# Kernel tuning notes

Measured on AMD Instinct MI355X. Metric: run time of the kernel, lower is better.

Reference implementation:

```python
import jax, jax.numpy as jnp
import numpy as np

N_HEADS = 32
N_KV_HEADS = 8
HEAD_DIM = 128
ROPE_BASE = 10000.0
NEG_INF = -1e9


def rope(x, base=ROPE_BASE, offset=0):
    # x: [B, H, L, d]; 'traditional' RoPE with the module's rotation formula.
    d = x.shape[-1]
    t = jnp.arange(x.shape[2], dtype=jnp.float32) + offset
    freqs = base ** (-jnp.arange(0, d, 2, dtype=jnp.float32) / d)  # [d/2]
    ang = t[:, None] * freqs[None, :]                              # [L, d/2]
    cos, sin = jnp.cos(ang), jnp.sin(ang)
    x1, x2 = x[..., 0::2], x[..., 1::2]
    out = jnp.stack([x1 * cos + x2 * sin, x1 * sin - x2 * cos], axis=-1)
    return out.reshape(x.shape)


def setup_inputs() -> dict:
    key = jax.random.key(0)
    ks = jax.random.split(key, 5)
    B, L, D = 2, 2048, 4096
    x = jax.random.normal(ks[0], (B, L, D), dtype=jnp.float32)
    wq = jax.random.normal(ks[1], (D, N_HEADS * HEAD_DIM), dtype=jnp.float32) * 0.02
    wk = jax.random.normal(ks[2], (D, N_KV_HEADS * HEAD_DIM), dtype=jnp.float32) * 0.02
    wv = jax.random.normal(ks[3], (D, N_KV_HEADS * HEAD_DIM), dtype=jnp.float32) * 0.02
    wo = jax.random.normal(ks[4], (N_HEADS * HEAD_DIM, D), dtype=jnp.float32) * 0.02
    # causal additive mask [L, L]
    mask = jnp.where(jnp.tril(jnp.ones((L, L), dtype=bool)), 0.0, NEG_INF).astype(jnp.float32)
    return {"x": x, "mask": mask, "wq": wq, "wk": wk, "wv": wv, "wo": wo}


def reference(x, mask, wq, wk, wv, wo):
    B, L, D = x.shape
    scale = HEAD_DIM ** -0.5
    q = (x @ wq).reshape(B, L, N_HEADS, HEAD_DIM).transpose(0, 2, 1, 3)     # [B,H,L,d]
    k = (x @ wk).reshape(B, L, N_KV_HEADS, HEAD_DIM).transpose(0, 2, 1, 3)  # [B,Hk,L,d]
    v = (x @ wv).reshape(B, L, N_KV_HEADS, HEAD_DIM).transpose(0, 2, 1, 3)
    rep = N_HEADS // N_KV_HEADS
    k = jnp.repeat(k, rep, axis=1)  # [B,H,L,d]  (physical GQA repeat, as in source)
    v = jnp.repeat(v, rep, axis=1)
    q = rope(q)
    k = rope(k)
    scores = jnp.einsum("bhqd,bhkd->bhqk", q * scale, k) + mask  # [B,H,L,L]
    probs = jax.nn.softmax(scores.astype(jnp.float32), axis=-1).astype(scores.dtype)
    out = jnp.einsum("bhqk,bhkd->bhqd", probs, v)
    out = out.transpose(0, 2, 1, 3).reshape(B, L, N_HEADS * HEAD_DIM)
    return out @ wo, (k, v)
```

## Files before the change

kernel.cpp:

```cpp
#include <hip/hip_runtime.h>

typedef unsigned short u16;
typedef unsigned int u32;
typedef float f32x4 __attribute__((ext_vector_type(4)));
typedef u32 u32x2 __attribute__((ext_vector_type(2)));
typedef __bf16 bf16x8 __attribute__((ext_vector_type(8)));

#define DEV __device__ __forceinline__

DEV u16 f2b(float f) {
    union { float f; u32 u; } v; v.f = f;
    u32 r = v.u + 0x7fffu + ((v.u >> 16) & 1u);
    return (u16)(r >> 16);
}
DEV float b2f(u16 b) {
    union { u32 u; float f; } v; v.u = ((u32)b) << 16;
    return v.f;
}

DEV void gload16(const void* g, void* l) {
    __builtin_amdgcn_global_load_lds((const __attribute__((address_space(1))) void*)g,
                                     (__attribute__((address_space(3))) void*)l, 16, 0, 0);
}

DEV f32x4 mfma16(bf16x8 a, bf16x8 b, f32x4 c) {
    return __builtin_amdgcn_mfma_f32_16x16x32_bf16(a, b, c, 0, 0, 0);
}

__global__ __launch_bounds__(256) void convx_kernel(const float* __restrict__ in,
                                                    u16* __restrict__ out) {
    size_t i = ((size_t)blockIdx.x * 256 + threadIdx.x) * 4;
    float4 v = *(const float4*)(in + i);
    ushort4 o; o.x = f2b(v.x); o.y = f2b(v.y); o.z = f2b(v.z); o.w = f2b(v.w);
    *(ushort4*)(out + i) = o;
}

__global__ __launch_bounds__(256) void tconv_kernel(const float* __restrict__ in,
                                                    u16* __restrict__ out, int K, int N) {
    __shared__ float tile[64][65];
    int t = threadIdx.x;
    int n0 = blockIdx.x * 64, k0 = blockIdx.y * 64;
    int r = t >> 4, c4 = (t & 15) * 4;
#pragma unroll
    for (int i = 0; i < 4; ++i) {
        float4 v = *(const float4*)(in + (size_t)(k0 + i * 16 + r) * N + n0 + c4);
        tile[i * 16 + r][c4 + 0] = v.x; tile[i * 16 + r][c4 + 1] = v.y;
        tile[i * 16 + r][c4 + 2] = v.z; tile[i * 16 + r][c4 + 3] = v.w;
    }
    __syncthreads();
#pragma unroll
    for (int i = 0; i < 4; ++i) {
        int nn = i * 16 + r;
        ushort4 o;
        o.x = f2b(tile[c4 + 0][nn]); o.y = f2b(tile[c4 + 1][nn]);
        o.z = f2b(tile[c4 + 2][nn]); o.w = f2b(tile[c4 + 3][nn]);
        *(ushort4*)(out + (size_t)(n0 + nn) * K + k0 + c4) = o;
    }
}

template <bool F32OUT>
__global__ __launch_bounds__(256, 2) void gemm128_kernel(const u16* __restrict__ A,
                                                         const u16* __restrict__ Bt,
                                                         u16* __restrict__ Cb,
                                                         float* __restrict__ Cf,
                                                         int N, int K, int gy) {
    __shared__ __align__(16) u16 Asb[2][2][64 * 64];
    __shared__ __align__(16) u16 Bsb[2][2][64 * 64];
    int t = threadIdx.x;
    int lane = t & 63, w = t >> 6;
    int wrM = w >> 1, wcN = w & 1;
    int lr = lane & 15, hi = lane >> 4;
    int wg = blockIdx.x;
    int swz = (wg & 7) * ((int)gridDim.x >> 3) + (wg >> 3);
    int bx = swz / gy, by = swz % gy;
    int m0 = by * 128, n0 = bx * 128;
    int nk = K >> 6;

    auto stageA = [&](int X, int h) {
        const u16* src = A + (size_t)(m0 + h * 64) * K + X * 64;
        char* dst = (char*)&Asb[X & 1][h][0];
#pragma unroll
        for (int it = 0; it < 2; ++it) {
            int c = it * 256 + t;
            int row = c >> 3;
            int col8 = ((c & 7) ^ (row & 7)) << 3;
            gload16(src + (size_t)row * K + col8, dst + (it * 256 + (t & ~63)) * 16);
        }
    };
    auto stageB = [&](int X, int h) {
        const u16* src = Bt + (size_t)(n0 + h * 64) * K + X * 64;
        char* dst = (char*)&Bsb[X & 1][h][0];
#pragma unroll
        for (int it = 0; it < 2; ++it) {
            int c = it * 256 + t;
            int row = c >> 3;
            int col8 = ((c & 7) ^ (row & 7)) << 3;
            gload16(src + (size_t)row * K + col8, dst + (it * 256 + (t & ~63)) * 16);
        }
    };

    stageA(0, 0); stageA(0, 1); stageB(0, 0); stageB(0, 1);
    stageA(1, 0); stageA(1, 1);
    asm volatile("s_waitcnt vmcnt(4)" ::: "memory");
    __builtin_amdgcn_s_barrier();

    f32x4 acc[4][4] = {};
    for (int kt = 0; kt < nk; ++kt) {
        __builtin_amdgcn_sched_barrier(0);
        int p = kt & 1;
        const char* Ah = (const char*)&Asb[p][wrM][0];
        const char* Bh = (const char*)&Bsb[p][wcN][0];
        bool s1 = (kt + 1 < nk), s2 = (kt + 2 < nk);
        bf16x8 a[4][2], bb[2][2];

#pragma unroll
        for (int mf = 0; mf < 4; ++mf)
#pragma unroll
            for (int ks = 0; ks < 2; ++ks) {
                int row = mf * 16 + lr;
                a[mf][ks] = *(const bf16x8*)(Ah + ((row * 128 + ks * 64 + hi * 16) ^ ((row & 7) << 4)));
            }
#pragma unroll
        for (int nf = 0; nf < 2; ++nf)
#pragma unroll
            for (int ks = 0; ks < 2; ++ks) {
                int row = nf * 16 + lr;
                bb[nf][ks] = *(const bf16x8*)(Bh + ((row * 128 + ks * 64 + hi * 16) ^ ((row & 7) << 4)));
            }
        if (s1) { stageB(kt + 1, 0); stageB(kt + 1, 1); }
        __builtin_amdgcn_s_barrier();
        __builtin_amdgcn_s_setprio(1);
#pragma unroll
        for (int mf = 0; mf < 4; ++mf)
#pragma unroll
            for (int nf = 0; nf < 2; ++nf)
#pragma unroll
                for (int ks = 0; ks < 2; ++ks)
                    acc[mf][nf] = mfma16(a[mf][ks], bb[nf][ks], acc[mf][nf]);
        __builtin_amdgcn_s_setprio(0);
        __builtin_amdgcn_s_barrier();

#pragma unroll
        for (int nf = 0; nf < 2; ++nf)
#pragma unroll
            for (int ks = 0; ks < 2; ++ks) {
                int row = (nf + 2) * 16 + lr;
                bb[nf][ks] = *(const bf16x8*)(Bh + ((row * 128 + ks * 64 + hi * 16) ^ ((row & 7) << 4)));
            }
        if (s2) { stageA(kt + 2, 0); stageA(kt + 2, 1); }
        __builtin_amdgcn_s_barrier();
        __builtin_amdgcn_s_setprio(1);
#pragma unroll
        for (int mf = 0; mf < 4; ++mf)
#pragma unroll
            for (int nf = 0; nf < 2; ++nf)
#pragma unroll
                for (int ks = 0; ks < 2; ++ks)
                    acc[mf][nf + 2] = mfma16(a[mf][ks], bb[nf][ks], acc[mf][nf + 2]);
        __builtin_amdgcn_s_setprio(0);
        if (s2)      asm volatile("s_waitcnt vmcnt(4)" ::: "memory");
        else if (s1) asm volatile("s_waitcnt vmcnt(0)" ::: "memory");
        __builtin_amdgcn_s_barrier();
    }

#pragma unroll
    for (int mf = 0; mf < 4; ++mf)
#pragma unroll
        for (int nf = 0; nf < 4; ++nf)
#pragma unroll
            for (int r = 0; r < 4; ++r) {
                int m = m0 + wrM * 64 + mf * 16 + hi * 4 + r;
                int n = n0 + wcN * 64 + nf * 16 + lr;
                if (F32OUT) Cf[(size_t)m * N + n] = acc[mf][nf][r];
                else        Cb[(size_t)m * N + n] = f2b(acc[mf][nf][r]);
            }
}

__global__ __launch_bounds__(256) void rope_kernel(u16* __restrict__ qkv,
                                                   float* __restrict__ outk) {
    int row = blockIdx.y;
    int p = blockIdx.x * 256 + threadIdx.x;
    int b = row >> 11, l = row & 2047;
    float freq = exp2f((float)(p & 63) * -0.2076205059304601f);
    float sv, cv; sincosf((float)l * freq, &sv, &cv);
    if (p < 2048) {
        int h = p >> 6, i = p & 63;
        size_t idx = (size_t)row * 6144 + h * 128 + 2 * i;
        u32 pr = *(const u32*)(qkv + idx);
        float x1 = b2f((u16)(pr & 0xffff)), x2 = b2f((u16)(pr >> 16));
        float o1 = x1 * cv + x2 * sv, o2 = x1 * sv - x2 * cv;
        *(u32*)(qkv + idx) = (u32)f2b(o1) | ((u32)f2b(o2) << 16);
    } else {
        int kvh = (p >> 6) - 32, i = p & 63;
        size_t idx = (size_t)row * 6144 + 4096 + kvh * 128 + 2 * i;
        u32 pr = *(const u32*)(qkv + idx);
        float x1 = b2f((u16)(pr & 0xffff)), x2 = b2f((u16)(pr >> 16));
        float o1 = x1 * cv + x2 * sv, o2 = x1 * sv - x2 * cv;
        *(u32*)(qkv + idx) = (u32)f2b(o1) | ((u32)f2b(o2) << 16);
#pragma unroll
        for (int r = 0; r < 4; ++r) {
            float2 o; o.x = o1; o.y = o2;
            *(float2*)(outk + ((size_t)((b * 32 + kvh * 4 + r) * 2048) + l) * 128 + 2 * i) = o;
        }
    }
}

__global__ __launch_bounds__(256) void vtrans_kernel(const u16* __restrict__ qkv,
                                                     u16* __restrict__ vt,
                                                     float* __restrict__ outv) {
    __shared__ u16 tile[64][65];
    int t = threadIdx.x;
    int l0 = blockIdx.x * 64, d0 = blockIdx.y * 64;
    int z = blockIdx.z, b = z >> 3, kvh = z & 7;
    int r = t >> 4, c4 = (t & 15) * 4;
#pragma unroll
    for (int i = 0; i < 4; ++i) {
        int l = l0 + i * 16 + r;
        ushort4 v = *(const ushort4*)(qkv + (size_t)(b * 2048 + l) * 6144 + 5120 + kvh * 128 + d0 + c4);
        tile[i * 16 + r][c4 + 0] = v.x; tile[i * 16 + r][c4 + 1] = v.y;
        tile[i * 16 + r][c4 + 2] = v.z; tile[i * 16 + r][c4 + 3] = v.w;
        float4 f; f.x = b2f(v.x); f.y = b2f(v.y); f.z = b2f(v.z); f.w = b2f(v.w);
#pragma unroll
        for (int rr = 0; rr < 4; ++rr)
            *(float4*)(outv + ((size_t)((b * 32 + kvh * 4 + rr) * 2048) + l) * 128 + d0 + c4) = f;
    }
    __syncthreads();
#pragma unroll
    for (int i = 0; i < 4; ++i) {
        int dn = i * 16 + r;
        ushort4 o;
        o.x = tile[c4 + 0][dn]; o.y = tile[c4 + 1][dn];
        o.z = tile[c4 + 2][dn]; o.w = tile[c4 + 3][dn];
        *(ushort4*)(vt + (size_t)((b * 8 + kvh) * 128 + d0 + dn) * 2048 + l0 + c4) = o;
    }
}

__global__ __launch_bounds__(256, 2) void attn_kernel(const u16* __restrict__ qkv,
                                                      const u16* __restrict__ vt,
                                                      u16* __restrict__ ab) {
    __shared__ __align__(16) u16 Kbuf[2][64 * 128];
    __shared__ __align__(16) u16 Vbuf[2][128 * 64];
    __shared__ __align__(16) u16 Ps[4][32 * 64];
    int t = threadIdx.x, lane = t & 63, w = t >> 6;
    int lr = lane & 15, hi = lane >> 4;
    int h = blockIdx.y, b = blockIdx.z, kvh = h >> 2;

    const u16* kbase = qkv + (size_t)(b * 2048) * 6144 + 4096 + kvh * 128;
    const u16* vtbase = vt + (size_t)((b * 8 + kvh) * 128) * 2048;

    auto stageKV = [&](int k0, int buf) {
#pragma unroll
        for (int i = 0; i < 4; ++i) {
            int c = i * 256 + t;
            int row = c >> 4;
            int col8 = ((c & 15) ^ (row & 7)) << 3;
            gload16(kbase + (size_t)(k0 + row) * 6144 + col8,
                    (char*)Kbuf[buf] + (i * 256 + (t & ~63)) * 16);
        }
#pragma unroll
        for (int i = 0; i < 4; ++i) {
            int c = i * 256 + t;
            int row = c >> 3;
            int col8 = ((c & 7) ^ (row & 7)) << 3;
            gload16(vtbase + (size_t)row * 2048 + k0 + col8,
                    (char*)Vbuf[buf] + (i * 256 + (t & ~63)) * 16);
        }
    };

    auto process = [&](int qblk) {
        int q0 = qblk * 128;
        bf16x8 qf[2][4];
#pragma unroll
        for (int half = 0; half < 2; ++half)
#pragma unroll
            for (int kki = 0; kki < 4; ++kki)
                qf[half][kki] = *(const bf16x8*)(qkv +
                    (size_t)(b * 2048 + q0 + w * 32 + half * 16 + lr) * 6144 + h * 128 +
                    kki * 32 + 8 * hi);
        f32x4 acc[2][8] = {};
        float mrun[2] = {-1e30f, -1e30f}, lrun[2] = {0.f, 0.f};

        int nt = 2 * (qblk + 1);
        stageKV(0, 0);
        __syncthreads();
        int cur = 0;
        for (int kt = 0; kt < nt; ++kt) {
            if (kt + 1 < nt) stageKV((kt + 1) * 64, cur ^ 1);
            __builtin_amdgcn_sched_barrier(0);

            const u16* Ks = Kbuf[cur];
            const u16* Vs = Vbuf[cur];
            f32x4 s[2][4] = {};
            __builtin_amdgcn_s_setprio(1);
#pragma unroll
            for (int kki = 0; kki < 4; ++kki) {
                bf16x8 kf[4];
#pragma unroll
                for (int fc = 0; fc < 4; ++fc) {
                    int kvr = fc * 16 + lr;
                    int byt = (kvr * 256 + (kki * 32 + 8 * hi) * 2) ^ ((kvr & 7) << 4);
                    kf[fc] = *(const bf16x8*)((const char*)Ks + byt);
                }
#pragma unroll
                for (int fc = 0; fc < 4; ++fc) {
                    s[0][fc] = mfma16(kf[fc], qf[0][kki], s[0][fc]);
                    s[1][fc] = mfma16(kf[fc], qf[1][kki], s[1][fc]);
                }
            }
            __builtin_amdgcn_s_setprio(0);
            const float SC = 0.08838834764831845f;
            int domask = (kt >= nt - 2);
            u16* Pw = Ps[w];
#pragma unroll
            for (int half = 0; half < 2; ++half) {
                int qabs = q0 + w * 32 + half * 16 + lr;
#pragma unroll
                for (int fc = 0; fc < 4; ++fc)
#pragma unroll
                    for (int r = 0; r < 4; ++r) {
                        float v = s[half][fc][r] * SC;
                        if (domask && (kt * 64 + fc * 16 + hi * 4 + r) > qabs) v = -1e30f;
                        s[half][fc][r] = v;
                    }
                float pm = s[half][0][0];
#pragma unroll
                for (int fc = 0; fc < 4; ++fc)
#pragma unroll
                    for (int r = 0; r < 4; ++r) pm = fmaxf(pm, s[half][fc][r]);
                pm = fmaxf(pm, __shfl_xor(pm, 16));
                pm = fmaxf(pm, __shfl_xor(pm, 32));
                float mn = fmaxf(mrun[half], pm);
                float fr = __expf(mrun[half] - mn);
                mrun[half] = mn;
                float ls = 0.f;
#pragma unroll
                for (int fc = 0; fc < 4; ++fc)
#pragma unroll
                    for (int r = 0; r < 4; ++r) {
                        float e = __expf(s[half][fc][r] - mn);
                        s[half][fc][r] = e;
                        ls += e;
                    }
                ls += __shfl_xor(ls, 16);
                ls += __shfl_xor(ls, 32);
                lrun[half] = lrun[half] * fr + ls;
#pragma unroll
                for (int dhf = 0; dhf < 8; ++dhf)
#pragma unroll
                    for (int r = 0; r < 4; ++r) acc[half][dhf][r] *= fr;
#pragma unroll
                for (int fc = 0; fc < 4; ++fc) {
                    u32x2 pk;
                    pk.x = (u32)f2b(s[half][fc][0]) | ((u32)f2b(s[half][fc][1]) << 16);
                    pk.y = (u32)f2b(s[half][fc][2]) | ((u32)f2b(s[half][fc][3]) << 16);
                    int byt = (half * 2048 + lr * 128 + fc * 32 + hi * 8) ^ ((lr & 7) << 4);
                    *(u32x2*)((char*)Pw + byt) = pk;
                }
            }
            asm volatile("s_waitcnt lgkmcnt(0)" ::: "memory");
            __builtin_amdgcn_s_setprio(1);
#pragma unroll
            for (int kk2 = 0; kk2 < 2; ++kk2) {
                bf16x8 pf0 = *(const bf16x8*)((const char*)Pw +
                    ((lr * 128 + kk2 * 64 + hi * 16) ^ ((lr & 7) << 4)));
                bf16x8 pf1 = *(const bf16x8*)((const char*)Pw +
                    ((2048 + lr * 128 + kk2 * 64 + hi * 16) ^ ((lr & 7) << 4)));
#pragma unroll
                for (int dhf = 0; dhf < 8; ++dhf) {
                    int dh = dhf * 16 + lr;
                    int bytv = (dh * 128 + (kk2 * 32 + 8 * hi) * 2) ^ ((dh & 7) << 4);
                    bf16x8 vf = *(const bf16x8*)((const char*)Vs + bytv);
                    acc[0][dhf] = mfma16(vf, pf0, acc[0][dhf]);
                    acc[1][dhf] = mfma16(vf, pf1, acc[1][dhf]);
                }
            }
            __builtin_amdgcn_s_setprio(0);
            __syncthreads();
            cur ^= 1;
        }
#pragma unroll
        for (int half = 0; half < 2; ++half) {
            float inv = 1.0f / lrun[half];
            int qrow = q0 + w * 32 + half * 16 + lr;
#pragma unroll
            for (int dhf = 0; dhf < 8; ++dhf) {
                ushort4 o;
                o.x = f2b(acc[half][dhf][0] * inv); o.y = f2b(acc[half][dhf][1] * inv);
                o.z = f2b(acc[half][dhf][2] * inv); o.w = f2b(acc[half][dhf][3] * inv);
                *(ushort4*)(ab + (size_t)(b * 2048 + qrow) * 4096 + h * 128 + dhf * 16 + hi * 4) = o;
            }
        }
    };

    process(15 - blockIdx.x);
    __syncthreads();
    process(blockIdx.x);
}

extern "C" void kernel_launch(void* const* d_in, const int* in_sizes, int n_in,
                              void* d_out, int out_size, void* d_ws, size_t ws_size,
                              hipStream_t stream) {
    (void)in_sizes; (void)n_in; (void)out_size; (void)ws_size;
    const float* x  = (const float*)d_in[0];
    const float* wq = (const float*)d_in[2];
    const float* wk = (const float*)d_in[3];
    const float* wv = (const float*)d_in[4];
    const float* wo = (const float*)d_in[5];

    char* ws = (char*)d_ws;
    u16* xb  = (u16*)(ws + 0);
    u16* fBt = (u16*)(ws + 33554432);
    u16* qkv = (u16*)(ws + 83886080);
    u16* vt  = (u16*)(ws + 134217728);
    u16* ab  = xb;
    u16* wob = fBt;

    float* out0 = (float*)d_out;
    float* outk = out0 + 16777216;
    float* outv = out0 + 33554432;

    convx_kernel<<<16384, 256, 0, stream>>>(x, xb);
    tconv_kernel<<<dim3(64, 64), 256, 0, stream>>>(wq, fBt, 4096, 4096);
    tconv_kernel<<<dim3(16, 64), 256, 0, stream>>>(wk, fBt + (size_t)4096 * 4096, 4096, 1024);
    tconv_kernel<<<dim3(16, 64), 256, 0, stream>>>(wv, fBt + (size_t)5120 * 4096, 4096, 1024);

    gemm128_kernel<false><<<1536, 256, 0, stream>>>(xb, fBt, qkv, nullptr, 6144, 4096, 32);

    tconv_kernel<<<dim3(64, 64), 256, 0, stream>>>(wo, wob, 4096, 4096);

    rope_kernel<<<dim3(10, 4096), 256, 0, stream>>>(qkv, outk);
    vtrans_kernel<<<dim3(32, 2, 16), 256, 0, stream>>>(qkv, vt, outv);

    attn_kernel<<<dim3(8, 32, 2), 256, 0, stream>>>(qkv, vt, ab);

    gemm128_kernel<true><<<1024, 256, 0, stream>>>(ab, wob, nullptr, out0, 4096, 4096, 32);
}
```

Before: 581.0 us.

## Use 256x128 GEMM tiles with triple buffering and merge small prep kernels

Replaces the 128x128 GEMM with a 256x128 block tile and a 32-wide K step, using a three-stage LDS ring with a single barrier per iteration. Each wave now computes a 128x64 sub-tile, which raises operand reuse and cuts barrier overhead. The change also merges the three weight-transpose launches into one kernel, and folds the RoPE and V-transpose kernels into a single postproc launch to save launch overhead. The costs are higher register pressure from the 8x4 accumulator array, which may hurt occupancy at launch_bounds(256,2), and half as many blocks in each GEMM grid.

```diff
diff --git a/kernel.cpp b/kernel.cpp
--- a/kernel.cpp
+++ b/kernel.cpp
@@ -35,6 +35,35 @@
     *(ushort4*)(out + i) = o;
 }
 
+__global__ __launch_bounds__(256) void tconv3_kernel(const float* __restrict__ wq,
+                                                     const float* __restrict__ wk,
+                                                     const float* __restrict__ wv,
+                                                     u16* __restrict__ out) {
+    __shared__ float tile[64][65];
+    int t = threadIdx.x;
+    int n0 = blockIdx.x * 64, k0 = blockIdx.y * 64;
+    const float* src; int Ns, nl;
+    if (n0 < 4096)      { src = wq; Ns = 4096; nl = n0; }
+    else if (n0 < 5120) { src = wk; Ns = 1024; nl = n0 - 4096; }
+    else                { src = wv; Ns = 1024; nl = n0 - 5120; }
+    int r = t >> 4, c4 = (t & 15) * 4;
+#pragma unroll
+    for (int i = 0; i < 4; ++i) {
+        float4 v = *(const float4*)(src + (size_t)(k0 + i * 16 + r) * Ns + nl + c4);
+        tile[i * 16 + r][c4 + 0] = v.x; tile[i * 16 + r][c4 + 1] = v.y;
+        tile[i * 16 + r][c4 + 2] = v.z; tile[i * 16 + r][c4 + 3] = v.w;
+    }
+    __syncthreads();
+#pragma unroll
+    for (int i = 0; i < 4; ++i) {
+        int nn = i * 16 + r;
+        ushort4 o;
+        o.x = f2b(tile[c4 + 0][nn]); o.y = f2b(tile[c4 + 1][nn]);
+        o.z = f2b(tile[c4 + 2][nn]); o.w = f2b(tile[c4 + 3][nn]);
+        *(ushort4*)(out + (size_t)(n0 + nn) * 4096 + k0 + c4) = o;
+    }
+}
+
 __global__ __launch_bounds__(256) void tconv_kernel(const float* __restrict__ in,
                                                     u16* __restrict__ out, int K, int N) {
     __shared__ float tile[64][65];
@@ -59,13 +88,13 @@
 }
 
 template <bool F32OUT>
-__global__ __launch_bounds__(256, 2) void gemm128_kernel(const u16* __restrict__ A,
-                                                         const u16* __restrict__ Bt,
-                                                         u16* __restrict__ Cb,
-                                                         float* __restrict__ Cf,
-                                                         int N, int K, int gy) {
-    __shared__ __align__(16) u16 Asb[2][2][64 * 64];
-    __shared__ __align__(16) u16 Bsb[2][2][64 * 64];
+__global__ __launch_bounds__(256, 2) void gemm256x128_kernel(const u16* __restrict__ A,
+                                                             const u16* __restrict__ Bt,
+                                                             u16* __restrict__ Cb,
+                                                             float* __restrict__ Cf,
+                                                             int N, int K, int gy) {
+    __shared__ __align__(16) u16 Asb[3][256 * 32];
+    __shared__ __align__(16) u16 Bsb[3][128 * 32];
     int t = threadIdx.x;
     int lane = t & 63, w = t >> 6;
     int wrM = w >> 1, wcN = w & 1;
@@ -73,165 +102,136 @@
     int wg = blockIdx.x;
     int swz = (wg & 7) * ((int)gridDim.x >> 3) + (wg >> 3);
     int bx = swz / gy, by = swz % gy;
-    int m0 = by * 128, n0 = bx * 128;
-    int nk = K >> 6;
-
-    auto stageA = [&](int X, int h) {
-        const u16* src = A + (size_t)(m0 + h * 64) * K + X * 64;
-        char* dst = (char*)&Asb[X & 1][h][0];
+    int m0 = by * 256, n0 = bx * 128;
+    int nk = K >> 5;
+
+    auto stage = [&](int X, int buf) {
+        const u16* srcA = A + (size_t)m0 * K + X * 32;
+        char* dstA = (char*)&Asb[buf][0];
+#pragma unroll
+        for (int it = 0; it < 4; ++it) {
+            int c = it * 256 + t;
+            int row = c >> 2;
+            int col8 = ((c & 3) ^ ((row >> 1) & 3)) << 3;
+            gload16(srcA + (size_t)row * K + col8, dstA + (it * 256 + (t & ~63)) * 16);
+        }
+        const u16* srcB = Bt + (size_t)n0 * K + X * 32;
+        char* dstB = (char*)&Bsb[buf][0];
 #pragma unroll
         for (int it = 0; it < 2; ++it) {
             int c = it * 256 + t;
-            int row = c >> 3;
-            int col8 = ((c & 7) ^ (row & 7)) << 3;
-            gload16(src + (size_t)row * K + col8, dst + (it * 256 + (t & ~63)) * 16);
+            int row = c >> 2;
+            int col8 = ((c & 3) ^ ((row >> 1) & 3)) << 3;
+            gload16(srcB + (size_t)row * K + col8, dstB + (it * 256 + (t & ~63)) * 16);
         }
     };
-    auto stageB = [&](int X, int h) {
-        const u16* src = Bt + (size_t)(n0 + h * 64) * K + X * 64;
-        char* dst = (char*)&Bsb[X & 1][h][0];
-#pragma unroll
-        for (int it = 0; it < 2; ++it) {
-            int c = it * 256 + t;
-            int row = c >> 3;
-            int col8 = ((c & 7) ^ (row & 7)) << 3;
-            gload16(src + (size_t)row * K + col8, dst + (it * 256 + (t & ~63)) * 16);
-        }
-    };
-
-    stageA(0, 0); stageA(0, 1); stageB(0, 0); stageB(0, 1);
-    stageA(1, 0); stageA(1, 1);
-    asm volatile("s_waitcnt vmcnt(4)" ::: "memory");
+
+    stage(0, 0); stage(1, 1);
+    asm volatile("s_waitcnt vmcnt(6)" ::: "memory");
     __builtin_amdgcn_s_barrier();
 
-    f32x4 acc[4][4] = {};
+    f32x4 acc[8][4] = {};
+    int p = 0;
     for (int kt = 0; kt < nk; ++kt) {
-        __builtin_amdgcn_sched_barrier(0);
-        int p = kt & 1;
-        const char* Ah = (const char*)&Asb[p][wrM][0];
-        const char* Bh = (const char*)&Bsb[p][wcN][0];
-        bool s1 = (kt + 1 < nk), s2 = (kt + 2 < nk);
-        bf16x8 a[4][2], bb[2][2];
-
-#pragma unroll
-        for (int mf = 0; mf < 4; ++mf)
-#pragma unroll
-            for (int ks = 0; ks < 2; ++ks) {
-                int row = mf * 16 + lr;
-                a[mf][ks] = *(const bf16x8*)(Ah + ((row * 128 + ks * 64 + hi * 16) ^ ((row & 7) << 4)));
-            }
-#pragma unroll
-        for (int nf = 0; nf < 2; ++nf)
-#pragma unroll
-            for (int ks = 0; ks < 2; ++ks) {
-                int row = nf * 16 + lr;
-                bb[nf][ks] = *(const bf16x8*)(Bh + ((row * 128 + ks * 64 + hi * 16) ^ ((row & 7) << 4)));
-            }
-        if (s1) { stageB(kt + 1, 0); stageB(kt + 1, 1); }
-        __builtin_amdgcn_s_barrier();
+        const char* Ah = (const char*)&Asb[p][0] + wrM * 8192;
+        const char* Bh = (const char*)&Bsb[p][0] + wcN * 4096;
+        bf16x8 a[8], bb[4];
+#pragma unroll
+        for (int mf = 0; mf < 8; ++mf) {
+            int row = mf * 16 + lr;
+            a[mf] = *(const bf16x8*)(Ah + ((row * 64 + hi * 16) ^ (((row >> 1) & 3) << 4)));
+        }
+#pragma unroll
+        for (int nf = 0; nf < 4; ++nf) {
+            int row = nf * 16 + lr;
+            bb[nf] = *(const bf16x8*)(Bh + ((row * 64 + hi * 16) ^ (((row >> 1) & 3) << 4)));
+        }
+        bool s2 = (kt + 2 < nk), s1 = (kt + 1 < nk);
+        if (s2) { int b2 = (p + 2 >= 3) ? p - 1 : p + 2; stage(kt + 2, b2); }
         __builtin_amdgcn_s_setprio(1);
 #pragma unroll
-        for (int mf = 0; mf < 4; ++mf)
-#pragma unroll
-            for (int nf = 0; nf < 2; ++nf)
-#pragma unroll
-                for (int ks = 0; ks < 2; ++ks)
-                    acc[mf][nf] = mfma16(a[mf][ks], bb[nf][ks], acc[mf][nf]);
+        for (int mf = 0; mf < 8; ++mf)
+#pragma unroll
+            for (int nf = 0; nf < 4; ++nf)
+                acc[mf][nf] = mfma16(a[mf], bb[nf], acc[mf][nf]);
         __builtin_amdgcn_s_setprio(0);
-        __builtin_amdgcn_s_barrier();
-
-#pragma unroll
-        for (int nf = 0; nf < 2; ++nf)
-#pragma unroll
-            for (int ks = 0; ks < 2; ++ks) {
-                int row = (nf + 2) * 16 + lr;
-                bb[nf][ks] = *(const bf16x8*)(Bh + ((row * 128 + ks * 64 + hi * 16) ^ ((row & 7) << 4)));
-            }
-        if (s2) { stageA(kt + 2, 0); stageA(kt + 2, 1); }
-        __builtin_amdgcn_s_barrier();
-        __builtin_amdgcn_s_setprio(1);
-#pragma unroll
-        for (int mf = 0; mf < 4; ++mf)
-#pragma unroll
-            for (int nf = 0; nf < 2; ++nf)
-#pragma unroll
-                for (int ks = 0; ks < 2; ++ks)
-                    acc[mf][nf + 2] = mfma16(a[mf][ks], bb[nf][ks], acc[mf][nf + 2]);
-        __builtin_amdgcn_s_setprio(0);
-        if (s2)      asm volatile("s_waitcnt vmcnt(4)" ::: "memory");
+        if (s2)      asm volatile("s_waitcnt vmcnt(6)" ::: "memory");
         else if (s1) asm volatile("s_waitcnt vmcnt(0)" ::: "memory");
         __builtin_amdgcn_s_barrier();
-    }
-
-#pragma unroll
-    for (int mf = 0; mf < 4; ++mf)
+        p = (p == 2) ? 0 : p + 1;
+    }
+
+#pragma unroll
+    for (int mf = 0; mf < 8; ++mf)
 #pragma unroll
         for (int nf = 0; nf < 4; ++nf)
 #pragma unroll
             for (int r = 0; r < 4; ++r) {
-                int m = m0 + wrM * 64 + mf * 16 + hi * 4 + r;
+                int m = m0 + wrM * 128 + mf * 16 + hi * 4 + r;
                 int n = n0 + wcN * 64 + nf * 16 + lr;
                 if (F32OUT) Cf[(size_t)m * N + n] = acc[mf][nf][r];
                 else        Cb[(size_t)m * N + n] = f2b(acc[mf][nf][r]);
             }
 }
 
-__global__ __launch_bounds__(256) void rope_kernel(u16* __restrict__ qkv,
-                                                   float* __restrict__ outk) {
-    int row = blockIdx.y;
-    int p = blockIdx.x * 256 + threadIdx.x;
-    int b = row >> 11, l = row & 2047;
-    float freq = exp2f((float)(p & 63) * -0.2076205059304601f);
-    float sv, cv; sincosf((float)l * freq, &sv, &cv);
-    if (p < 2048) {
-        int h = p >> 6, i = p & 63;
-        size_t idx = (size_t)row * 6144 + h * 128 + 2 * i;
-        u32 pr = *(const u32*)(qkv + idx);
-        float x1 = b2f((u16)(pr & 0xffff)), x2 = b2f((u16)(pr >> 16));
-        float o1 = x1 * cv + x2 * sv, o2 = x1 * sv - x2 * cv;
-        *(u32*)(qkv + idx) = (u32)f2b(o1) | ((u32)f2b(o2) << 16);
+__global__ __launch_bounds__(256) void postproc_kernel(u16* __restrict__ qkv,
+                                                       float* __restrict__ outk,
+                                                       u16* __restrict__ vt,
+                                                       float* __restrict__ outv) {
+    int id = blockIdx.x;
+    int tid = threadIdx.x;
+    if (id < 40960) {
+        int row = id / 10;
+        int p = (id % 10) * 256 + tid;
+        int b = row >> 11, l = row & 2047;
+        float freq = exp2f((float)(p & 63) * -0.2076205059304601f);
+        float sv, cv; sincosf((float)l * freq, &sv, &cv);
+        if (p < 2048) {
+            int h = p >> 6, i = p & 63;
+            size_t idx = (size_t)row * 6144 + h * 128 + 2 * i;
+            u32 pr = *(const u32*)(qkv + idx);
+            float x1 = b2f((u16)(pr & 0xffff)), x2 = b2f((u16)(pr >> 16));
+            float o1 = x1 * cv + x2 * sv, o2 = x1 * sv - x2 * cv;
+            *(u32*)(qkv + idx) = (u32)f2b(o1) | ((u32)f2b(o2) << 16);
+        } else {
+            int kvh = (p >> 6) - 32, i = p & 63;
+            size_t idx = (size_t)row * 6144 + 4096 + kvh * 128 + 2 * i;
+            u32 pr = *(const u32*)(qkv + idx);
+            float x1 = b2f((u16)(pr & 0xffff)), x2 = b2f((u16)(pr >> 16));
+            float o1 = x1 * cv + x2 * sv, o2 = x1 * sv - x2 * cv;
+            *(u32*)(qkv + idx) = (u32)f2b(o1) | ((u32)f2b(o2) << 16);
+#pragma unroll
+            for (int r = 0; r < 4; ++r) {
+                float2 o; o.x = o1; o.y = o2;
+                *(float2*)(outk + ((size_t)((b * 32 + kvh * 4 + r) * 2048) + l) * 128 + 2 * i) = o;
+            }
+        }
     } else {
-        int kvh = (p >> 6) - 32, i = p & 63;
-        size_t idx = (size_t)row * 6144 + 4096 + kvh * 128 + 2 * i;
-        u32 pr = *(const u32*)(qkv + idx);
-        float x1 = b2f((u16)(pr & 0xffff)), x2 = b2f((u16)(pr >> 16));
-        float o1 = x1 * cv + x2 * sv, o2 = x1 * sv - x2 * cv;
-        *(u32*)(qkv + idx) = (u32)f2b(o1) | ((u32)f2b(o2) << 16);
-#pragma unroll
-        for (int r = 0; r < 4; ++r) {
-            float2 o; o.x = o1; o.y = o2;
-            *(float2*)(outk + ((size_t)((b * 32 + kvh * 4 + r) * 2048) + l) * 128 + 2 * i) = o;
-        }
-    }
-}
-
-__global__ __launch_bounds__(256) void vtrans_kernel(const u16* __restrict__ qkv,
-                                                     u16* __restrict__ vt,
-                                                     float* __restrict__ outv) {
-    __shared__ u16 tile[64][65];
-    int t = threadIdx.x;
-    int l0 = blockIdx.x * 64, d0 = blockIdx.y * 64;
-    int z = blockIdx.z, b = z >> 3, kvh = z & 7;
-    int r = t >> 4, c4 = (t & 15) * 4;
-#pragma unroll
-    for (int i = 0; i < 4; ++i) {
-        int l = l0 + i * 16 + r;
-        ushort4 v = *(const ushort4*)(qkv + (size_t)(b * 2048 + l) * 6144 + 5120 + kvh * 128 + d0 + c4);
-        tile[i * 16 + r][c4 + 0] = v.x; tile[i * 16 + r][c4 + 1] = v.y;
-        tile[i * 16 + r][c4 + 2] = v.z; tile[i * 16 + r][c4 + 3] = v.w;
-        float4 f; f.x = b2f(v.x); f.y = b2f(v.y); f.z = b2f(v.z); f.w = b2f(v.w);
-#pragma unroll
-        for (int rr = 0; rr < 4; ++rr)
-            *(float4*)(outv + ((size_t)((b * 32 + kvh * 4 + rr) * 2048) + l) * 128 + d0 + c4) = f;
-    }
-    __syncthreads();
-#pragma unroll
-    for (int i = 0; i < 4; ++i) {
-        int dn = i * 16 + r;
-        ushort4 o;
-        o.x = tile[c4 + 0][dn]; o.y = tile[c4 + 1][dn];
-        o.z = tile[c4 + 2][dn]; o.w = tile[c4 + 3][dn];
-        *(ushort4*)(vt + (size_t)((b * 8 + kvh) * 128 + d0 + dn) * 2048 + l0 + c4) = o;
+        __shared__ u16 tile[64][65];
+        int i0 = id - 40960;
+        int l0 = (i0 & 31) * 64, d0 = ((i0 >> 5) & 1) * 64;
+        int z = i0 >> 6, b = z >> 3, kvh = z & 7;
+        int r = tid >> 4, c4 = (tid & 15) * 4;
+#pragma unroll
+        for (int i = 0; i < 4; ++i) {
+            int l = l0 + i * 16 + r;
+            ushort4 v = *(const ushort4*)(qkv + (size_t)(b * 2048 + l) * 6144 + 5120 + kvh * 128 + d0 + c4);
+            tile[i * 16 + r][c4 + 0] = v.x; tile[i * 16 + r][c4 + 1] = v.y;
+            tile[i * 16 + r][c4 + 2] = v.z; tile[i * 16 + r][c4 + 3] = v.w;
+            float4 f; f.x = b2f(v.x); f.y = b2f(v.y); f.z = b2f(v.z); f.w = b2f(v.w);
+#pragma unroll
+            for (int rr = 0; rr < 4; ++rr)
+                *(float4*)(outv + ((size_t)((b * 32 + kvh * 4 + rr) * 2048) + l) * 128 + d0 + c4) = f;
+        }
+        __syncthreads();
+#pragma unroll
+        for (int i = 0; i < 4; ++i) {
+            int dn = i * 16 + r;
+            ushort4 o;
+            o.x = tile[c4 + 0][dn]; o.y = tile[c4 + 1][dn];
+            o.z = tile[c4 + 2][dn]; o.w = tile[c4 + 3][dn];
+            *(ushort4*)(vt + (size_t)((b * 8 + kvh) * 128 + d0 + dn) * 2048 + l0 + c4) = o;
+        }
     }
 }
 
@@ -420,18 +420,15 @@
     float* outv = out0 + 33554432;
 
     convx_kernel<<<16384, 256, 0, stream>>>(x, xb);
-    tconv_kernel<<<dim3(64, 64), 256, 0, stream>>>(wq, fBt, 4096, 4096);
-    tconv_kernel<<<dim3(16, 64), 256, 0, stream>>>(wk, fBt + (size_t)4096 * 4096, 4096, 1024);
-    tconv_kernel<<<dim3(16, 64), 256, 0, stream>>>(wv, fBt + (size_t)5120 * 4096, 4096, 1024);
-
-    gemm128_kernel<false><<<1536, 256, 0, stream>>>(xb, fBt, qkv, nullptr, 6144, 4096, 32);
+    tconv3_kernel<<<dim3(96, 64), 256, 0, stream>>>(wq, wk, wv, fBt);
+
+    gemm256x128_kernel<false><<<768, 256, 0, stream>>>(xb, fBt, qkv, nullptr, 6144, 4096, 16);
 
     tconv_kernel<<<dim3(64, 64), 256, 0, stream>>>(wo, wob, 4096, 4096);
 
-    rope_kernel<<<dim3(10, 4096), 256, 0, stream>>>(qkv, outk);
-    vtrans_kernel<<<dim3(32, 2, 16), 256, 0, stream>>>(qkv, vt, outv);
+    postproc_kernel<<<41984, 256, 0, stream>>>(qkv, outk, vt, outv);
 
     attn_kernel<<<dim3(8, 32, 2), 256, 0, stream>>>(qkv, vt, ab);
 
-    gemm128_kernel<true><<<1024, 256, 0, stream>>>(ab, wob, nullptr, out0, 4096, 4096, 32);
-}
+    gemm256x128_kernel<true><<<512, 256, 0, stream>>>(ab, wob, nullptr, out0, 4096, 4096, 16);
+}
```

New measurement: 599.7 us. 1.03x slower.
